# Performance work log

Measured on AMD Instinct MI355X. Metric: run time of the kernel, lower is better.

Reference implementation:

```python
import jax, jax.numpy as jnp
import numpy as np

DIM = 64
HID = 512
BATCH = 8192
W_SCALE = 0.05  # keeps alpha small so exp(alpha) stays stable over 64 sequential steps


def _build_masks(dim, hid, seed=0):
    # Faithful to MADE.create_masks: degrees m[-1]=m[1]=arange(dim), m[0]=randint(0,dim-1,hid)
    rng = np.random.RandomState(seed)
    m_in = np.arange(dim)
    m0 = rng.randint(0, dim - 1, size=hid)
    mask1 = (m_in[:, None] <= m0[None, :]).T.astype(np.float32)          # [hid, dim]
    base = (m0[:, None] < m_in[None, :]).T                               # [dim, hid]
    mask2 = np.repeat(base, 2, axis=0).astype(np.float32)                # [2*dim, hid]
    return mask1, mask2


def setup_inputs() -> dict:
    key = jax.random.key(0)
    kz, kw1, kb1, kw2, kb2 = jax.random.split(key, 5)
    mask1, mask2 = _build_masks(DIM, HID)
    return {
        "z": jax.random.normal(kz, (BATCH, DIM), dtype=jnp.float32),
        "W1": jax.random.normal(kw1, (HID, DIM), dtype=jnp.float32) * W_SCALE,
        "b1": jax.random.normal(kb1, (HID,), dtype=jnp.float32) * W_SCALE,
        "W2": jax.random.normal(kw2, (2 * DIM, HID), dtype=jnp.float32) * W_SCALE,
        "b2": jax.random.normal(kb2, (2 * DIM,), dtype=jnp.float32) * W_SCALE,
        "mask1": jnp.asarray(mask1),
        "mask2": jnp.asarray(mask2),
    }


def _made(x, W1, b1, W2, b2, mask1, mask2):
    # MaskedLinear: linear(x, mask*W, b); two layers with ReLU between
    h = jax.nn.relu(x @ (mask1 * W1).T + b1)      # [B, hid]
    return h @ (mask2 * W2).T + b2                # [B, 2*dim] -> chunk: mu=[:dim], alpha=[dim:]


def reference(z, W1, b1, W2, b2, mask1, mask2):
    dim = z.shape[1]

    def step(x, i):
        params = _made(x, W1, b1, W2, b2, mask1, mask2)
        mu_i = params[:, i]            # mu = params[:, :dim]
        alpha_i = params[:, dim + i]   # alpha = params[:, dim:]
        x = x.at[:, i].set(z[:, i] * jnp.exp(alpha_i) + mu_i)
        return x, None

    x, _ = jax.lax.scan(step, jnp.zeros_like(z), jnp.arange(dim))
    final_params = _made(x, W1, b1, W2, b2, mask1, mask2)
    log_det_jacobian = jnp.sum(final_params[:, dim:], axis=1)
    return x, log_det_jacobian
```

## Files before the change

kernel.cpp:

```cpp
#include <hip/hip_runtime.h>
#include <math.h>

#define DIM   64
#define HID   512
#define BATCH 8192
#define R     2
#define REC   1536

#define W2SUM_OFF (64 * REC)
#define B2SUM_OFF (W2SUM_OFF + HID)
#define WS_FLOATS (B2SUM_OFF + 1)

typedef float f32x4 __attribute__((ext_vector_type(4)));
typedef float f32x2 __attribute__((ext_vector_type(2)));

__global__ void prep_kernel(const float* __restrict__ W1,
                            const float* __restrict__ mask1,
                            const float* __restrict__ W2,
                            const float* __restrict__ mask2,
                            const float* __restrict__ b2,
                            float* __restrict__ ws) {
    int t = blockIdx.x * blockDim.x + threadIdx.x;
    const int nrec = 64 * REC;
    if (t < nrec) {
        int rec = t / REC;
        int pos = t - rec * REC;
        float v;
        if (pos < HID) {
            int j = pos;
            v = mask2[rec * HID + j] * W2[rec * HID + j];
        } else if (pos < 2 * HID) {
            int j = pos - HID;
            v = mask2[(DIM + rec) * HID + j] * W2[(DIM + rec) * HID + j];
        } else {
            int j = pos - 2 * HID;
            v = mask1[j * DIM + rec] * W1[j * DIM + rec];
        }
        ws[t] = v;
    } else if (t < nrec + HID) {
        int j = t - nrec;
        float s = 0.f;
        for (int r = 0; r < DIM; ++r) {
            int idx = (DIM + r) * HID + j;
            s += mask2[idx] * W2[idx];
        }
        ws[W2SUM_OFF + j] = s;
    } else if (t == nrec + HID) {
        float s = 0.f;
        for (int r = 0; r < DIM; ++r) s += b2[DIM + r];
        ws[B2SUM_OFF] = s;
    }
}

__device__ __forceinline__ float wave_sum_dpp(float x) {
    x += __int_as_float(__builtin_amdgcn_update_dpp(0, __float_as_int(x), 0x111, 0xf, 0xf, true));
    x += __int_as_float(__builtin_amdgcn_update_dpp(0, __float_as_int(x), 0x112, 0xf, 0xf, true));
    x += __int_as_float(__builtin_amdgcn_update_dpp(0, __float_as_int(x), 0x114, 0xf, 0xf, true));
    x += __int_as_float(__builtin_amdgcn_update_dpp(0, __float_as_int(x), 0x118, 0xf, 0xf, true));
    x += __int_as_float(__builtin_amdgcn_update_dpp(0, __float_as_int(x), 0x142, 0xa, 0xf, true));
    x += __int_as_float(__builtin_amdgcn_update_dpp(0, __float_as_int(x), 0x143, 0xc, 0xf, true));
    return x;
}

__device__ __forceinline__ float readlane_f(float v, int lane) {
    return __int_as_float(__builtin_amdgcn_readlane(__float_as_int(v), lane));
}

__global__ __launch_bounds__(256, 4) void maf_kernel(
    const float* __restrict__ z,
    const float* __restrict__ b1,
    const float* __restrict__ b2,
    const float* __restrict__ ws,
    float* __restrict__ out) {
    const int lane = threadIdx.x & 63;
    const int wid  = (blockIdx.x * blockDim.x + threadIdx.x) >> 6;
    const int b0   = wid * R;
    const f32x4 Z4 = {0.f, 0.f, 0.f, 0.f};

    f32x4 h[R][2];
    {
        f32x4 bv0 = *(const f32x4*)(b1 + lane * 8);
        f32x4 bv1 = *(const f32x4*)(b1 + lane * 8 + 4);
#pragma unroll
        for (int r = 0; r < R; ++r) { h[r][0] = bv0; h[r][1] = bv1; }
    }
    float zl[R];
#pragma unroll
    for (int r = 0; r < R; ++r) zl[r] = z[(b0 + r) * DIM + lane];
    const float b2lo = b2[lane];
    const float b2hi = b2[DIM + lane];
    float xm[R];
#pragma unroll
    for (int r = 0; r < R; ++r) xm[r] = 0.f;

#define LOADW(p, M0, M1, A0, A1, C0, C1)                                    \
    do {                                                                    \
        M0 = *(const f32x4*)((p) - 512); M1 = *(const f32x4*)((p) - 508);   \
        A0 = *(const f32x4*)(p);         A1 = *(const f32x4*)((p) + 4);     \
        C0 = *(const f32x4*)((p) + 512); C1 = *(const f32x4*)((p) + 516);   \
    } while (0)

#define STEP(i, M0, M1, A0, A1, C0, C1)                                     \
    do {                                                                    \
        float _pm[R], _pa[R];                                               \
        _Pragma("unroll")                                                   \
        for (int r = 0; r < R; ++r) {                                       \
            f32x4 r0 = __builtin_elementwise_max(h[r][0], Z4);              \
            f32x4 r1 = __builtin_elementwise_max(h[r][1], Z4);              \
            f32x4 am = r0 * M0 + r1 * M1;                                   \
            f32x4 aa = r0 * A0 + r1 * A1;                                   \
            f32x2 tm = __builtin_shufflevector(am, am, 0, 1)                \
                     + __builtin_shufflevector(am, am, 2, 3);               \
            f32x2 ta = __builtin_shufflevector(aa, aa, 0, 1)                \
                     + __builtin_shufflevector(aa, aa, 2, 3);               \
            _pm[r] = wave_sum_dpp(tm.x + tm.y);                             \
            _pa[r] = wave_sum_dpp(ta.x + ta.y);                             \
        }                                                                   \
        const float _b2i  = readlane_f(b2lo, (i));                          \
        const float _b2di = readlane_f(b2hi, (i));                          \
        const bool  _at   = (lane == (i));                                  \
        _Pragma("unroll")                                                   \
        for (int r = 0; r < R; ++r) {                                       \
            const float _zi = readlane_f(zl[r], (i));                       \
            float _xv = _zi * __expf(_pa[r] + _b2di) + (_pm[r] + _b2i);     \
            const float _xs = readlane_f(_xv, 63);                          \
            if (_at) xm[r] = _xs;                                           \
            h[r][0] += C0 * _xs;                                            \
            h[r][1] += C1 * _xs;                                            \
        }                                                                   \
    } while (0)

    f32x4 m0A, m1A, a0A, a1A, c0A, c1A;
    f32x4 m0B, m1B, a0B, a1B, c0B, c1B;

    const float* wp = ws + HID + lane * 8;
    LOADW(wp, m0A, m1A, a0A, a1A, c0A, c1A);
    wp += REC;

#pragma unroll 1
    for (int i = 0; i < 62; i += 2) {
        LOADW(wp, m0B, m1B, a0B, a1B, c0B, c1B);
        __builtin_amdgcn_s_barrier();
        STEP(i, m0A, m1A, a0A, a1A, c0A, c1A);
        const float* wq = wp + REC;
        LOADW(wq, m0A, m1A, a0A, a1A, c0A, c1A);
        STEP(i + 1, m0B, m1B, a0B, a1B, c0B, c1B);
        wp = wq + REC;
    }
    LOADW(wp, m0B, m1B, a0B, a1B, c0B, c1B);
    STEP(62, m0A, m1A, a0A, a1A, c0A, c1A);
    STEP(63, m0B, m1B, a0B, a1B, c0B, c1B);

    const float* w2s = ws + W2SUM_OFF;
    f32x4 s0 = *(const f32x4*)(w2s + lane * 8);
    f32x4 s1 = *(const f32x4*)(w2s + lane * 8 + 4);
    const float bsum = ws[B2SUM_OFF];
#pragma unroll
    for (int r = 0; r < R; ++r) {
        out[(b0 + r) * DIM + lane] = xm[r];
        f32x4 acc = __builtin_elementwise_max(h[r][0], Z4) * s0
                  + __builtin_elementwise_max(h[r][1], Z4) * s1;
        f32x2 t = __builtin_shufflevector(acc, acc, 0, 1)
                + __builtin_shufflevector(acc, acc, 2, 3);
        float pl = wave_sum_dpp(t.x + t.y);
        if (lane == 63) out[BATCH * DIM + b0 + r] = pl + bsum;
    }
#undef LOADW
#undef STEP
}

extern "C" void kernel_launch(void* const* d_in, const int* in_sizes, int n_in,
                              void* d_out, int out_size, void* d_ws, size_t ws_size,
                              hipStream_t stream) {
    const float* z     = (const float*)d_in[0];
    const float* W1    = (const float*)d_in[1];
    const float* b1    = (const float*)d_in[2];
    const float* W2    = (const float*)d_in[3];
    const float* b2    = (const float*)d_in[4];
    const float* mask1 = (const float*)d_in[5];
    const float* mask2 = (const float*)d_in[6];
    float* out = (float*)d_out;
    float* ws  = (float*)d_ws;

    {
        int total  = WS_FLOATS;
        int blocks = (total + 255) / 256;
        prep_kernel<<<blocks, 256, 0, stream>>>(W1, mask1, W2, mask2, b2, ws);
    }
    {
        int threads = 256;
        int blocks  = BATCH / (R * 4);
        maf_kernel<<<blocks, threads, 0, stream>>>(z, b1, b2, ws, out);
    }
}
```

Before: 75.74 us.

## Process four batch rows per wave with packed FP32 FMA inline asm

Each wave now handles four batch rows instead of two, so every weight vector loaded per step is reused across more rows and the grid shrinks to half as many blocks. The inner dot products and the hidden-state updates are rewritten with explicit v_pk_mul_f32/v_pk_fma_f32 inline assembly on float2 pairs, meant to halve the VALU instruction count. Launch bounds drop from 4 to 2 blocks per SM to leave room for the doubled register state. The cost is lower occupancy and fewer waves overall to hide the latency of the sequential 64-step chain, and the inline asm may limit how freely the compiler can schedule.

Measured after the change: 77.63 us. +2.5%, slower.

```diff
diff --git a/kernel.cpp b/kernel.cpp
--- a/kernel.cpp
+++ b/kernel.cpp
@@ -4,7 +4,7 @@
 #define DIM   64
 #define HID   512
 #define BATCH 8192
-#define R     2
+#define R     4
 #define REC   1536
 
 #define W2SUM_OFF (64 * REC)
@@ -52,6 +52,19 @@
     }
 }
 
+__device__ __forceinline__ f32x2 pk_fma(f32x2 a, f32x2 b, f32x2 c) {
+    f32x2 d;
+    asm("v_pk_fma_f32 %0, %1, %2, %3" : "=v"(d) : "v"(a), "v"(b), "v"(c));
+    return d;
+}
+__device__ __forceinline__ f32x2 pk_mul(f32x2 a, f32x2 b) {
+    f32x2 d;
+    asm("v_pk_mul_f32 %0, %1, %2" : "=v"(d) : "v"(a), "v"(b));
+    return d;
+}
+__device__ __forceinline__ f32x2 lo2(f32x4 v) { return __builtin_shufflevector(v, v, 0, 1); }
+__device__ __forceinline__ f32x2 hi2(f32x4 v) { return __builtin_shufflevector(v, v, 2, 3); }
+
 __device__ __forceinline__ float wave_sum_dpp(float x) {
     x += __int_as_float(__builtin_amdgcn_update_dpp(0, __float_as_int(x), 0x111, 0xf, 0xf, true));
     x += __int_as_float(__builtin_amdgcn_update_dpp(0, __float_as_int(x), 0x112, 0xf, 0xf, true));
@@ -66,7 +79,7 @@
     return __int_as_float(__builtin_amdgcn_readlane(__float_as_int(v), lane));
 }
 
-__global__ __launch_bounds__(256, 4) void maf_kernel(
+__global__ __launch_bounds__(256, 2) void maf_kernel(
     const float* __restrict__ z,
     const float* __restrict__ b1,
     const float* __restrict__ b2,
@@ -75,14 +88,17 @@
     const int lane = threadIdx.x & 63;
     const int wid  = (blockIdx.x * blockDim.x + threadIdx.x) >> 6;
     const int b0   = wid * R;
-    const f32x4 Z4 = {0.f, 0.f, 0.f, 0.f};
-
-    f32x4 h[R][2];
+    const f32x2 Z2 = {0.f, 0.f};
+
+    f32x2 h[R][4];
     {
         f32x4 bv0 = *(const f32x4*)(b1 + lane * 8);
         f32x4 bv1 = *(const f32x4*)(b1 + lane * 8 + 4);
 #pragma unroll
-        for (int r = 0; r < R; ++r) { h[r][0] = bv0; h[r][1] = bv1; }
+        for (int r = 0; r < R; ++r) {
+            h[r][0] = lo2(bv0); h[r][1] = hi2(bv0);
+            h[r][2] = lo2(bv1); h[r][3] = hi2(bv1);
+        }
     }
     float zl[R];
 #pragma unroll
@@ -105,16 +121,20 @@
         float _pm[R], _pa[R];                                               \
         _Pragma("unroll")                                                   \
         for (int r = 0; r < R; ++r) {                                       \
-            f32x4 r0 = __builtin_elementwise_max(h[r][0], Z4);              \
-            f32x4 r1 = __builtin_elementwise_max(h[r][1], Z4);              \
-            f32x4 am = r0 * M0 + r1 * M1;                                   \
-            f32x4 aa = r0 * A0 + r1 * A1;                                   \
-            f32x2 tm = __builtin_shufflevector(am, am, 0, 1)                \
-                     + __builtin_shufflevector(am, am, 2, 3);               \
-            f32x2 ta = __builtin_shufflevector(aa, aa, 0, 1)                \
-                     + __builtin_shufflevector(aa, aa, 2, 3);               \
-            _pm[r] = wave_sum_dpp(tm.x + tm.y);                             \
-            _pa[r] = wave_sum_dpp(ta.x + ta.y);                             \
+            f32x2 q0 = __builtin_elementwise_max(h[r][0], Z2);              \
+            f32x2 q1 = __builtin_elementwise_max(h[r][1], Z2);              \
+            f32x2 q2 = __builtin_elementwise_max(h[r][2], Z2);              \
+            f32x2 q3 = __builtin_elementwise_max(h[r][3], Z2);              \
+            f32x2 am = pk_mul(q0, lo2(M0));                                 \
+            am = pk_fma(q1, hi2(M0), am);                                   \
+            am = pk_fma(q2, lo2(M1), am);                                   \
+            am = pk_fma(q3, hi2(M1), am);                                   \
+            f32x2 aa = pk_mul(q0, lo2(A0));                                 \
+            aa = pk_fma(q1, hi2(A0), aa);                                   \
+            aa = pk_fma(q2, lo2(A1), aa);                                   \
+            aa = pk_fma(q3, hi2(A1), aa);                                   \
+            _pm[r] = wave_sum_dpp(am.x + am.y);                             \
+            _pa[r] = wave_sum_dpp(aa.x + aa.y);                             \
         }                                                                   \
         const float _b2i  = readlane_f(b2lo, (i));                          \
         const float _b2di = readlane_f(b2hi, (i));                          \
@@ -125,8 +145,11 @@
             float _xv = _zi * __expf(_pa[r] + _b2di) + (_pm[r] + _b2i);     \
             const float _xs = readlane_f(_xv, 63);                          \
             if (_at) xm[r] = _xs;                                           \
-            h[r][0] += C0 * _xs;                                            \
-            h[r][1] += C1 * _xs;                                            \
+            f32x2 _xs2 = {_xs, _xs};                                        \
+            h[r][0] = pk_fma(lo2(C0), _xs2, h[r][0]);                       \
+            h[r][1] = pk_fma(hi2(C0), _xs2, h[r][1]);                       \
+            h[r][2] = pk_fma(lo2(C1), _xs2, h[r][2]);                       \
+            h[r][3] = pk_fma(hi2(C1), _xs2, h[r][3]);                       \
         }                                                                   \
     } while (0)
 
@@ -158,11 +181,11 @@
 #pragma unroll
     for (int r = 0; r < R; ++r) {
         out[(b0 + r) * DIM + lane] = xm[r];
-        f32x4 acc = __builtin_elementwise_max(h[r][0], Z4) * s0
-                  + __builtin_elementwise_max(h[r][1], Z4) * s1;
-        f32x2 t = __builtin_shufflevector(acc, acc, 0, 1)
-                + __builtin_shufflevector(acc, acc, 2, 3);
-        float pl = wave_sum_dpp(t.x + t.y);
+        f32x2 acc = pk_mul(__builtin_elementwise_max(h[r][0], Z2), lo2(s0));
+        acc = pk_fma(__builtin_elementwise_max(h[r][1], Z2), hi2(s0), acc);
+        acc = pk_fma(__builtin_elementwise_max(h[r][2], Z2), lo2(s1), acc);
+        acc = pk_fma(__builtin_elementwise_max(h[r][3], Z2), hi2(s1), acc);
+        float pl = wave_sum_dpp(acc.x + acc.y);
         if (lane == 63) out[BATCH * DIM + b0 + r] = pl + bsum;
     }
 #undef LOADW
```
